# Kernel optimization log

Measured on AMD Instinct MI355X. Metric: run time of the kernel, lower is better.

## Reference

```python
import jax, jax.numpy as jnp
import numpy as np

N_HEAD = 16
D_HEAD = 64


def setup_inputs() -> dict:
    key = jax.random.key(0)
    k1, k2, k3, k4 = jax.random.split(key, 4)
    T, B, D = 1024, 8, 1024
    input = jax.random.normal(k1, (T, B, D), dtype=jnp.float32)
    pos_enc = jax.random.normal(k2, (T, B, D), dtype=jnp.float32) * 0.1
    # causal mask: True = masked (future positions), broadcast over batch
    causal = jnp.triu(jnp.ones((T, T), dtype=bool), k=1)
    attn_mask = jnp.broadcast_to(causal[None, :, :], (B, T, T))
    W_qkv = jax.random.normal(k3, (D, 3 * N_HEAD * D_HEAD), dtype=jnp.float32) * (D ** -0.5)
    W_o = jax.random.normal(k4, (N_HEAD * D_HEAD, N_HEAD * D_HEAD), dtype=jnp.float32) * ((N_HEAD * D_HEAD) ** -0.5)
    return {"input": input, "pos_enc": pos_enc, "attn_mask": attn_mask,
            "W_qkv": W_qkv, "W_o": W_o}


def reference(input, pos_enc, attn_mask, W_qkv, W_o):
    T, B, D = input.shape
    scale = 1.0 / (D_HEAD ** 0.5)
    # attn_type == 2: qkv on (w + r)
    heads = (input + pos_enc) @ W_qkv                      # [T,B,3*n*d]
    q, k, v = jnp.split(heads, 3, axis=-1)
    q = q.reshape(T, B, N_HEAD, D_HEAD)
    k = k.reshape(T, B, N_HEAD, D_HEAD)
    v = v.reshape(T, B, N_HEAD, D_HEAD)
    # scores [B, n, qlen, klen]
    score = jnp.einsum('ibnd,jbnd->bnij', q, k) * scale
    score = jnp.where(attn_mask[:, None, :, :], -jnp.inf, score)
    prob = jax.nn.softmax(score.astype(jnp.float32), axis=-1)  # [B,n,i,j]
    # coverage: mean over heads -> [B,i,j], then transpose -> [B,j,i]
    coverage = jnp.mean(prob, axis=1).transpose(0, 2, 1)
    # dropout is identity at eval (dropatt=0)
    attn_vec = jnp.einsum('bnij,jbnd->ibnd', prob, v)       # [T,B,n,d]
    attn_vec = attn_vec.reshape(T, B, N_HEAD * D_HEAD)
    attn_out = attn_vec @ W_o
    return attn_out, coverage
```

## Files before the change

### kernel.cpp

```cpp
#include <hip/hip_runtime.h>
#include <hip/hip_bf16.h>


typedef __bf16 v8bf __attribute__((ext_vector_type(8)));
typedef float  v4f  __attribute__((ext_vector_type(4)));
typedef unsigned short v8us __attribute__((ext_vector_type(8)));

#define MFMA16x16x32(a, b, c) __builtin_amdgcn_mfma_f32_16x16x32_bf16(a, b, c, 0, 0, 0)

#define GLD_LDS16(g, l) \
    __builtin_amdgcn_global_load_lds((const __attribute__((address_space(1))) void*)(g), \
                                     (__attribute__((address_space(3))) void*)(l), 16, 0, 0)

__device__ __forceinline__ unsigned short f2bf(float f) {
    unsigned int u = __float_as_uint(f);
    u = (u + 0x7FFF + ((u >> 16) & 1)) >> 16;
    return (unsigned short)u;
}

__global__ __launch_bounds__(256) void prep_x(const float* __restrict__ in,
                                              const float* __restrict__ pe,
                                              unsigned short* __restrict__ x) {
    size_t idx = ((size_t)blockIdx.x * 256 + threadIdx.x) * 8;
    v4f a0 = *(const v4f*)(in + idx);
    v4f a1 = *(const v4f*)(in + idx + 4);
    v4f p0 = *(const v4f*)(pe + idx);
    v4f p1 = *(const v4f*)(pe + idx + 4);
    v8us r;
    unsigned short* rp = (unsigned short*)&r;
#pragma unroll
    for (int q = 0; q < 4; q++) {
        rp[q]     = f2bf(a0[q] + p0[q]);
        rp[q + 4] = f2bf(a1[q] + p1[q]);
    }
    *(v8us*)(x + idx) = r;
}

__global__ __launch_bounds__(256) void transpose_f32_bf16(const float* __restrict__ src,
                                                          unsigned short* __restrict__ dst,
                                                          int R, int C) {
    __shared__ alignas(16) unsigned short t[64][72];
    int c0 = blockIdx.x * 64, r0 = blockIdx.y * 64;
    int tid = threadIdx.x;
    int rr = tid >> 2, cg = (tid & 3) * 16;
    const float* s = src + (size_t)(r0 + rr) * C + c0 + cg;
#pragma unroll
    for (int q4 = 0; q4 < 4; q4++) {
        v4f v = *(const v4f*)(s + q4 * 4);
#pragma unroll
        for (int q = 0; q < 4; q++) t[rr][cg + q4 * 4 + q] = f2bf(v[q]);
    }
    __syncthreads();
    v8us o0, o1;
    unsigned short* o0p = (unsigned short*)&o0;
    unsigned short* o1p = (unsigned short*)&o1;
#pragma unroll
    for (int q = 0; q < 8; q++) {
        o0p[q] = t[cg + q][rr];
        o1p[q] = t[cg + 8 + q][rr];
    }
    *(v8us*)(dst + (size_t)(c0 + rr) * R + r0 + cg)     = o0;
    *(v8us*)(dst + (size_t)(c0 + rr) * R + r0 + cg + 8) = o1;
}

__global__ __launch_bounds__(256) void transpose_v(const unsigned short* __restrict__ heads,
                                                   unsigned short* __restrict__ Vt) {
    __shared__ alignas(16) unsigned short t[64][72];
    const int bn = blockIdx.y, b = bn >> 4, n = bn & 15;
    const int j0 = blockIdx.x * 64;
    const int tid = threadIdx.x;
    const int jr = tid >> 2, dg = (tid & 3) * 16;
    const unsigned short* s = heads + ((size_t)(j0 + jr) * 8 + b) * 3072 + 2048 + n * 64 + dg;
    *(v8us*)&t[jr][dg]     = *(const v8us*)(s);
    *(v8us*)&t[jr][dg + 8] = *(const v8us*)(s + 8);
    __syncthreads();
    const int dr = tid >> 2, jg = (tid & 3) * 16;
    v8us o0, o1;
    unsigned short* o0p = (unsigned short*)&o0;
    unsigned short* o1p = (unsigned short*)&o1;
#pragma unroll
    for (int q = 0; q < 8; q++) {
        o0p[q] = t[jg + q][dr];
        o1p[q] = t[jg + 8 + q][dr];
    }
    unsigned short* d = Vt + ((size_t)bn * 64 + dr) * 1024 + j0 + jg;
    *(v8us*)(d)     = o0;
    *(v8us*)(d + 8) = o1;
}

template <bool F32OUT>
__global__ __launch_bounds__(256) void gemm_bf16_v2(const unsigned short* __restrict__ A,
                                                    const unsigned short* __restrict__ Bt,
                                                    void* __restrict__ Cout,
                                                    int M, int N, int K) {
    __shared__ alignas(16) unsigned short As[128 * 64];
    __shared__ alignas(16) unsigned short Bs[128 * 64];

    const int nwgx = gridDim.x;
    const int id   = blockIdx.y * nwgx + blockIdx.x;
    const int cpx  = (nwgx * gridDim.y) >> 3;
    const int id2  = (id & 7) * cpx + (id >> 3);
    const int m0 = (id2 / nwgx) * 128, n0 = (id2 % nwgx) * 128;

    const int tid = threadIdx.x;
    const int lane = tid & 63, wave = tid >> 6;
    const int quad = lane >> 4, lq = lane & 15, lq7 = lq & 7;
    const int mW = (wave & 1) * 64, nW = (wave >> 1) * 64;

    v4f acc[4][4];
#pragma unroll
    for (int mi = 0; mi < 4; mi++)
#pragma unroll
        for (int ni = 0; ni < 4; ni++) acc[mi][ni] = (v4f){0.f, 0.f, 0.f, 0.f};

    const int lr = lane >> 3, lu = lane & 7;
    const int ug = lu ^ lr;
    const unsigned short* agl = A  + (size_t)(m0 + wave * 32 + lr) * K + ug * 8;
    const unsigned short* bgl = Bt + (size_t)(n0 + wave * 32 + lr) * K + ug * 8;
    unsigned short* AsW = (unsigned short*)As + wave * 32 * 64;
    unsigned short* BsW = (unsigned short*)Bs + wave * 32 * 64;

    for (int k0 = 0; k0 < K; k0 += 64) {
        __syncthreads();
#pragma unroll
        for (int t = 0; t < 4; t++) {
            GLD_LDS16(agl + k0 + (size_t)t * 8 * K, AsW + t * 512);
            GLD_LDS16(bgl + k0 + (size_t)t * 8 * K, BsW + t * 512);
        }
        __syncthreads();
#pragma unroll
        for (int h = 0; h < 2; h++) {
            v8bf af[4], bfr[4];
#pragma unroll
            for (int mi = 0; mi < 4; mi++)
                af[mi] = *(const v8bf*)&As[(mW + mi * 16 + lq) * 64 + (((quad + 4 * h) ^ lq7) * 8)];
#pragma unroll
            for (int ni = 0; ni < 4; ni++)
                bfr[ni] = *(const v8bf*)&Bs[(nW + ni * 16 + lq) * 64 + (((quad + 4 * h) ^ lq7) * 8)];
#pragma unroll
            for (int mi = 0; mi < 4; mi++)
#pragma unroll
                for (int ni = 0; ni < 4; ni++)
                    acc[mi][ni] = MFMA16x16x32(af[mi], bfr[ni], acc[mi][ni]);
        }
    }

#pragma unroll
    for (int mi = 0; mi < 4; mi++)
#pragma unroll
        for (int ni = 0; ni < 4; ni++)
#pragma unroll
            for (int r = 0; r < 4; r++) {
                int row = m0 + mW + mi * 16 + quad * 4 + r;
                int col = n0 + nW + ni * 16 + lq;
                if (F32OUT)
                    ((float*)Cout)[(size_t)row * N + col] = acc[mi][ni][r];
                else
                    ((unsigned short*)Cout)[(size_t)row * N + col] = f2bf(acc[mi][ni][r]);
            }
}

#define AT_T  1024
#define AT_B  8
#define AT_NH 16
#define AT_HS 3072
#define AT_ALPHA 0.18033688011112042f

__global__ __launch_bounds__(256) void attn_fused5(const unsigned short* __restrict__ heads,
                                                   const unsigned short* __restrict__ Vt,
                                                   unsigned short* __restrict__ av,
                                                   float* __restrict__ lBuf) {
    __shared__ alignas(16) unsigned short KL[64 * 64];
    __shared__ alignas(16) unsigned short VL[64 * 64];
    __shared__ alignas(16) unsigned short Ps[4 * 16 * 32];
    const int bn = blockIdx.x, b = bn >> 4, n = bn & 15;
    const int y = blockIdx.y;
    const int g = (y < 8) ? (15 - y) : (y - 8);
    const int tid = threadIdx.x;
    const int wv = tid >> 6, lane = tid & 63;
    const int quad = lane >> 4, lq = lane & 15;
    const int i0 = g * 64 + wv * 16;
    const int imax = i0 + 15;

    size_t qbase = ((size_t)(i0 + lq) * 8 + b) * AT_HS + n * 64 + quad * 8;
    v8bf q0 = *(const v8bf*)(heads + qbase);
    v8bf q1 = *(const v8bf*)(heads + qbase + 32);

    const int srow = tid >> 3, sunit = tid & 7;
    const size_t kRowStride = (size_t)8 * AT_HS;
    const unsigned short* kg = heads + ((size_t)srow * 8 + b) * AT_HS + 1024 + n * 64 + sunit * 8;
    const unsigned short* vg = Vt + ((size_t)bn * 64 + srow) * 1024 + sunit * 8;
    const int swz = ((sunit ^ (srow & 7)) * 8);
    unsigned short* kw0 = KL + srow * 64 + swz;
    unsigned short* kw1 = KL + (srow + 32) * 64 + swz;
    unsigned short* vw0 = VL + srow * 64 + swz;
    unsigned short* vw1 = VL + (srow + 32) * 64 + swz;

    v8us kr0 = *(const v8us*)(kg);
    v8us kr1 = *(const v8us*)(kg + 32 * kRowStride);
    v8us vr0 = *(const v8us*)(vg);
    v8us vr1 = *(const v8us*)(vg + 32 * 1024);

    unsigned short* psw = Ps + wv * 512;
    const v8bf* pr = (const v8bf*)(psw + lq * 32 + ((quad ^ (lq & 3)) * 8));
    const int lq7 = lq & 7, lqh = lq >> 3;

    float Sl[4] = {0.f, 0.f, 0.f, 0.f};
    v4f o[4];
#pragma unroll
    for (int dt = 0; dt < 4; dt++) o[dt] = (v4f){0.f, 0.f, 0.f, 0.f};

    for (int c = 0; c <= g; ++c) {
        __syncthreads();
        *(v8us*)kw0 = kr0; *(v8us*)kw1 = kr1;
        *(v8us*)vw0 = vr0; *(v8us*)vw1 = vr1;
        __syncthreads();
        if (c < g) {
            const unsigned short* kgn = kg + (size_t)(c + 1) * 64 * kRowStride;
            kr0 = *(const v8us*)(kgn);
            kr1 = *(const v8us*)(kgn + 32 * kRowStride);
            const unsigned short* vgn = vg + (c + 1) * 64;
            vr0 = *(const v8us*)(vgn);
            vr1 = *(const v8us*)(vgn + 32 * 1024);
        }
        const int jb = c * 64;
#pragma unroll
        for (int jj = 0; jj < 64; jj += 32) {
            const int j0 = jb + jj;
            if (j0 <= imax) {
                const v8bf ka = *(const v8bf*)(KL + (jj + lq) * 64      + ((quad ^ lq7) * 8));
                const v8bf kb = *(const v8bf*)(KL + (jj + lq) * 64      + (((4 + quad) ^ lq7) * 8));
                const v8bf kc = *(const v8bf*)(KL + (jj + 16 + lq) * 64 + ((quad ^ lq7) * 8));
                const v8bf kd = *(const v8bf*)(KL + (jj + 16 + lq) * 64 + (((4 + quad) ^ lq7) * 8));
                v4f s0 = (v4f){0.f, 0.f, 0.f, 0.f}, s1 = s0;
                s0 = MFMA16x16x32(q0, ka, s0);
                s0 = MFMA16x16x32(q1, kb, s0);
                s1 = MFMA16x16x32(q0, kc, s1);
                s1 = MFMA16x16x32(q1, kd, s1);
                const int ja = j0 + lq, jb2 = j0 + 16 + lq;
#pragma unroll
                for (int r = 0; r < 4; ++r) {
                    const int i = i0 + quad * 4 + r;
                    float e0 = exp2f(s0[r] * AT_ALPHA);
                    float e1 = exp2f(s1[r] * AT_ALPHA);
                    float p0 = (ja  <= i) ? e0 : 0.f;
                    float p1 = (jb2 <= i) ? e1 : 0.f;
                    Sl[r] += p0 + p1;
                    psw[(quad * 4 + r) * 32 + ((lqh ^ r) * 8) + lq7]        = f2bf(p0);
                    psw[(quad * 4 + r) * 32 + (((lqh | 2) ^ r) * 8) + lq7]  = f2bf(p1);
                }
                const v8bf pf = *pr;
#pragma unroll
                for (int dt = 0; dt < 4; ++dt) {
                    const v8bf vf = *(const v8bf*)(VL + (dt * 16 + lq) * 64 +
                                                   ((((jj >> 3) + quad) ^ lq7) * 8));
                    o[dt] = MFMA16x16x32(pf, vf, o[dt]);
                }
            }
        }
    }

#pragma unroll
    for (int mask = 1; mask < 16; mask <<= 1)
#pragma unroll
        for (int r = 0; r < 4; r++)
            Sl[r] += __shfl_xor(Sl[r], mask);
    float linv[4];
#pragma unroll
    for (int r = 0; r < 4; r++) linv[r] = __builtin_amdgcn_rcpf(Sl[r]);
    if (lq == 0) {
#pragma unroll
        for (int r = 0; r < 4; r++) {
            int i = i0 + quad * 4 + r;
            lBuf[(size_t)bn * AT_T + i] = Sl[r];
        }
    }
#pragma unroll
    for (int dt = 0; dt < 4; dt++)
#pragma unroll
        for (int r = 0; r < 4; r++) {
            int i = i0 + quad * 4 + r;
            av[((size_t)i * 8 + b) * 1024 + n * 64 + dt * 16 + lq] = f2bf(o[dt][r] * linv[r]);
        }
}

__global__ __launch_bounds__(256) void coverage3(const unsigned short* __restrict__ heads,
                                                 const float* __restrict__ lBuf,
                                                 float* __restrict__ cov) {
    const int jt64 = blockIdx.x, it64 = blockIdx.y, b = blockIdx.z;
    const int i0 = it64 * 64, j0 = jt64 * 64;
    const int tid = threadIdx.x;

    if (jt64 > it64) {
        float* base = cov + (size_t)b * 1048576 + (size_t)(j0 + (tid >> 2)) * 1024
                      + i0 + (tid & 3) * 16;
        v4f z = (v4f){0.f, 0.f, 0.f, 0.f};
#pragma unroll
        for (int q = 0; q < 4; q++) *(v4f*)(base + q * 4) = z;
        return;
    }

    __shared__ alignas(16) char smem[64 * 68 * 4];
    unsigned short* QL = (unsigned short*)smem;
    unsigned short* KL = (unsigned short*)(smem + 8192);
    float* TF = (float*)smem;

    const int wv = tid >> 6, lane = tid & 63;
    const int quad = lane >> 4, lq = lane & 15, lq7 = lq & 7;
    const bool diag = (it64 == jt64);
    const int jtmax = diag ? wv : 3;

    const int srow = tid >> 3, sunit = tid & 7;
    const unsigned short* qgb = heads + ((size_t)(i0 + srow) * 8 + b) * AT_HS + sunit * 8;
    const unsigned short* kgb = heads + ((size_t)(j0 + srow) * 8 + b) * AT_HS + 1024 + sunit * 8;
    const int rowOff32 = 32 * 8 * AT_HS;
    const int swz = (sunit ^ (srow & 7)) * 8;
    unsigned short* qw0 = QL + srow * 64 + swz;
    unsigned short* qw1 = QL + (srow + 32) * 64 + swz;
    unsigned short* kw0 = KL + srow * 64 + swz;
    unsigned short* kw1 = KL + (srow + 32) * 64 + swz;

    v8us qr0 = *(const v8us*)(qgb);
    v8us qr1 = *(const v8us*)(qgb + rowOff32);
    v8us kr0 = *(const v8us*)(kgb);
    v8us kr1 = *(const v8us*)(kgb + rowOff32);

    v4f acc[4];
#pragma unroll
    for (int jt = 0; jt < 4; jt++) acc[jt] = (v4f){0.f, 0.f, 0.f, 0.f};

    const float* lrow = lBuf + (size_t)b * 16 * AT_T + i0 + wv * 16 + quad * 4;

    for (int n = 0; n < 16; ++n) {
        __syncthreads();
        *(v8us*)qw0 = qr0; *(v8us*)qw1 = qr1;
        *(v8us*)kw0 = kr0; *(v8us*)kw1 = kr1;
        __syncthreads();
        if (n < 15) {
            qr0 = *(const v8us*)(qgb + (n + 1) * 64);
            qr1 = *(const v8us*)(qgb + (n + 1) * 64 + rowOff32);
            kr0 = *(const v8us*)(kgb + (n + 1) * 64);
            kr1 = *(const v8us*)(kgb + (n + 1) * 64 + rowOff32);
        }
        v4f lv = *(const v4f*)(lrow + (size_t)n * AT_T);
        float linv[4];
#pragma unroll
        for (int r = 0; r < 4; r++) linv[r] = __builtin_amdgcn_rcpf(lv[r]);

        const v8bf qa = *(const v8bf*)(QL + (wv * 16 + lq) * 64 + ((quad ^ lq7) * 8));
        const v8bf qb = *(const v8bf*)(QL + (wv * 16 + lq) * 64 + (((4 + quad) ^ lq7) * 8));
#pragma unroll
        for (int jt = 0; jt < 4; jt++) {
            if (jt <= jtmax) {
                const v8bf ka = *(const v8bf*)(KL + (jt * 16 + lq) * 64 + ((quad ^ lq7) * 8));
                const v8bf kb = *(const v8bf*)(KL + (jt * 16 + lq) * 64 + (((4 + quad) ^ lq7) * 8));
                v4f s = (v4f){0.f, 0.f, 0.f, 0.f};
                s = MFMA16x16x32(qa, ka, s);
                s = MFMA16x16x32(qb, kb, s);
#pragma unroll
                for (int r = 0; r < 4; r++) {
                    float e = exp2f(s[r] * AT_ALPHA);
                    if (diag && jt == wv && lq > quad * 4 + r) e = 0.f;
                    acc[jt][r] = fmaf(e, linv[r], acc[jt][r]);
                }
            }
        }
    }

    __syncthreads();
#pragma unroll
    for (int jt = 0; jt < 4; jt++) {
        v4f w = acc[jt] * 0.0625f;
        *(v4f*)(TF + (size_t)(jt * 16 + lq) * 68 + wv * 16 + quad * 4) = w;
    }
    __syncthreads();
    {
        const int jl = tid >> 2, cg = (tid & 3) * 16;
        float* dst = cov + (size_t)b * 1048576 + (size_t)(j0 + jl) * 1024 + i0 + cg;
        const float* src = TF + (size_t)jl * 68 + cg;
#pragma unroll
        for (int q = 0; q < 4; q++) *(v4f*)(dst + q * 4) = *(const v4f*)(src + q * 4);
    }
}

extern "C" void kernel_launch(void* const* d_in, const int* in_sizes, int n_in,
                              void* d_out, int out_size, void* d_ws, size_t ws_size,
                              hipStream_t stream) {
    const float* input = (const float*)d_in[0];
    const float* pos   = (const float*)d_in[1];
    const float* Wqkv  = (const float*)d_in[3];
    const float* Wo    = (const float*)d_in[4];
    float* out = (float*)d_out;

    char* ws = (char*)d_ws;
    if (ws_size < 93323264) return;
    unsigned short* x     = (unsigned short*)(ws);
    unsigned short* heads = (unsigned short*)(ws + 16777216);
    unsigned short* av    = (unsigned short*)(ws + 67108864);
    unsigned short* WqkvT = (unsigned short*)(ws + 83886080);
    unsigned short* WoT   = (unsigned short*)(ws + 90177536);
    float* lBuf = (float*)(ws + 92798976);
    unsigned short* Vt = x;

    prep_x<<<4096, 256, 0, stream>>>(input, pos, x);
    transpose_f32_bf16<<<dim3(48, 16), 256, 0, stream>>>(Wqkv, WqkvT, 1024, 3072);
    transpose_f32_bf16<<<dim3(16, 16), 256, 0, stream>>>(Wo, WoT, 1024, 1024);
    gemm_bf16_v2<false><<<dim3(24, 64), 256, 0, stream>>>(x, WqkvT, heads, 8192, 3072, 1024);
    transpose_v<<<dim3(16, 128), 256, 0, stream>>>(heads, Vt);
    attn_fused5<<<dim3(128, 16), 256, 0, stream>>>(heads, Vt, av, lBuf);
    coverage3<<<dim3(16, 16, 8), 256, 0, stream>>>(heads, lBuf, out + 8388608);
    gemm_bf16_v2<true><<<dim3(8, 64), 256, 0, stream>>>(av, WoT, out, 8192, 1024, 1024);
}
```

Measured before the change: 337.8 us.

## Use 256x256 double-buffered GEMM tile for QKV projection

Adds a new GEMM kernel with 256x256 output tiles, 512 threads and double-buffered LDS staging through direct global-to-LDS loads, and uses it for the QKV projection. The larger tile raises arithmetic intensity and cuts redundant global loads, and double-buffering overlaps the next K-tile load with the MFMA work. In exchange it uses 128KB of LDS per block and many accumulator registers, which lowers occupancy. The grid also shrinks to 384 blocks, which may leave CUs unevenly loaded.

Result: slower. 350.9 us (+3.9%).

```diff
diff --git a/kernel.cpp b/kernel.cpp
--- a/kernel.cpp
+++ b/kernel.cpp
@@ -89,6 +89,113 @@
 }
 
 template <bool F32OUT>
+__global__ __launch_bounds__(512, 2) void gemm_bf16_256(const unsigned short* __restrict__ A,
+                                                        const unsigned short* __restrict__ Bt,
+                                                        void* __restrict__ Cout,
+                                                        int M, int N, int K) {
+    __shared__ alignas(16) unsigned short As[2][256 * 64];
+    __shared__ alignas(16) unsigned short Bs[2][256 * 64];
+
+    const int nwgx = gridDim.x;
+    const int id   = blockIdx.y * nwgx + blockIdx.x;
+    const int cpx  = (nwgx * gridDim.y) >> 3;
+    const int id2  = (id & 7) * cpx + (id >> 3);
+    const int m0 = (id2 / nwgx) * 256, n0 = (id2 % nwgx) * 256;
+
+    const int tid = threadIdx.x;
+    const int wv = tid >> 6, lane = tid & 63;
+    const int wm = wv >> 2, wn = wv & 3;
+    const int quad = lane >> 4, lq = lane & 15, lq7 = lq & 7;
+
+    v4f acc[8][4];
+#pragma unroll
+    for (int mf = 0; mf < 8; mf++)
+#pragma unroll
+        for (int nf = 0; nf < 4; nf++) acc[mf][nf] = (v4f){0.f, 0.f, 0.f, 0.f};
+
+    const int lr = lane >> 3, lu = lane & 7;
+    const int ug = lu ^ lr;
+    const unsigned short* agl = A  + (size_t)(m0 + wv * 32 + lr) * K + ug * 8;
+    const unsigned short* bgl = Bt + (size_t)(n0 + wv * 32 + lr) * K + ug * 8;
+
+#define STAGE256(buf, kk)                                                          \
+    do {                                                                           \
+        _Pragma("unroll")                                                          \
+        for (int t = 0; t < 4; t++) {                                              \
+            GLD_LDS16(agl + (size_t)(kk) * 64 + (size_t)t * 8 * K,                 \
+                      &As[buf][(wv * 32 + t * 8) * 64]);                           \
+            GLD_LDS16(bgl + (size_t)(kk) * 64 + (size_t)t * 8 * K,                 \
+                      &Bs[buf][(wv * 32 + t * 8) * 64]);                           \
+        }                                                                          \
+    } while (0)
+
+    const int NT = K >> 6;
+    STAGE256(0, 0);
+    STAGE256(1, 1);
+
+    for (int t2 = 0; t2 < NT; ++t2) {
+        const int c = t2 & 1;
+        if (t2 + 1 < NT) asm volatile("s_waitcnt vmcnt(8)" ::: "memory");
+        else             asm volatile("s_waitcnt vmcnt(0)" ::: "memory");
+        __builtin_amdgcn_sched_barrier(0);
+        __builtin_amdgcn_s_barrier();
+        __builtin_amdgcn_sched_barrier(0);
+
+#pragma unroll
+        for (int qm = 0; qm < 2; qm++) {
+            v8bf af[4][2];
+#pragma unroll
+            for (int mf = 0; mf < 4; mf++)
+#pragma unroll
+                for (int kh = 0; kh < 2; kh++)
+                    af[mf][kh] = *(const v8bf*)&As[c][(wm * 128 + (qm * 4 + mf) * 16 + lq) * 64 +
+                                                      (((kh * 4 + quad) ^ lq7) * 8)];
+#pragma unroll
+            for (int qn = 0; qn < 2; qn++) {
+                v8bf bfr[2][2];
+#pragma unroll
+                for (int nf = 0; nf < 2; nf++)
+#pragma unroll
+                    for (int kh = 0; kh < 2; kh++)
+                        bfr[nf][kh] = *(const v8bf*)&Bs[c][(wn * 64 + (qn * 2 + nf) * 16 + lq) * 64 +
+                                                           (((kh * 4 + quad) ^ lq7) * 8)];
+                __builtin_amdgcn_s_setprio(1);
+#pragma unroll
+                for (int mf = 0; mf < 4; mf++)
+#pragma unroll
+                    for (int nf = 0; nf < 2; nf++)
+#pragma unroll
+                        for (int kh = 0; kh < 2; kh++)
+                            acc[qm * 4 + mf][qn * 2 + nf] =
+                                MFMA16x16x32(af[mf][kh], bfr[nf][kh], acc[qm * 4 + mf][qn * 2 + nf]);
+                __builtin_amdgcn_s_setprio(0);
+            }
+        }
+
+        asm volatile("" ::: "memory");
+        __builtin_amdgcn_sched_barrier(0);
+        __builtin_amdgcn_s_barrier();
+        __builtin_amdgcn_sched_barrier(0);
+        if (t2 + 2 < NT) STAGE256(c, t2 + 2);
+    }
+
+#pragma unroll
+    for (int mf = 0; mf < 8; mf++)
+#pragma unroll
+        for (int nf = 0; nf < 4; nf++)
+#pragma unroll
+            for (int r = 0; r < 4; r++) {
+                int row = m0 + wm * 128 + mf * 16 + quad * 4 + r;
+                int col = n0 + wn * 64 + nf * 16 + lq;
+                if (F32OUT)
+                    ((float*)Cout)[(size_t)row * N + col] = acc[mf][nf][r];
+                else
+                    ((unsigned short*)Cout)[(size_t)row * N + col] = f2bf(acc[mf][nf][r]);
+            }
+#undef STAGE256
+}
+
+template <bool F32OUT>
 __global__ __launch_bounds__(256) void gemm_bf16_v2(const unsigned short* __restrict__ A,
                                                     const unsigned short* __restrict__ Bt,
                                                     void* __restrict__ Cout,
@@ -405,7 +512,7 @@
     prep_x<<<4096, 256, 0, stream>>>(input, pos, x);
     transpose_f32_bf16<<<dim3(48, 16), 256, 0, stream>>>(Wqkv, WqkvT, 1024, 3072);
     transpose_f32_bf16<<<dim3(16, 16), 256, 0, stream>>>(Wo, WoT, 1024, 1024);
-    gemm_bf16_v2<false><<<dim3(24, 64), 256, 0, stream>>>(x, WqkvT, heads, 8192, 3072, 1024);
+    gemm_bf16_256<false><<<dim3(12, 32), 512, 0, stream>>>(x, WqkvT, heads, 8192, 3072, 1024);
     transpose_v<<<dim3(16, 128), 256, 0, stream>>>(heads, Vt);
     attn_fused5<<<dim3(128, 16), 256, 0, stream>>>(heads, Vt, av, lBuf);
     coverage3<<<dim3(16, 16, 8), 256, 0, stream>>>(heads, lBuf, out + 8388608);
```

## Merge prep kernels into one launch and co-schedule coverage with output GEMM

Applied to the files above, without the earlier changes.

Three preprocessing kernels (input+pos cast, two weight transposes) are merged into one launch that dispatches on block index. The coverage kernel and the final W_o GEMM become a single launch, with blocks partitioned by flat index. The goal is to cut launch overhead and fill idle CUs during the lightly loaded coverage tail by running the independent GEMM work at the same time. In exchange, the combined kernel carries the larger of the two register and LDS footprints, which may lower occupancy for the coverage blocks.

Result: slower. 353.5 us (+4.6%).

```diff
diff --git a/kernel.cpp b/kernel.cpp
--- a/kernel.cpp
+++ b/kernel.cpp
@@ -18,30 +18,11 @@
     return (unsigned short)u;
 }
 
-__global__ __launch_bounds__(256) void prep_x(const float* __restrict__ in,
-                                              const float* __restrict__ pe,
-                                              unsigned short* __restrict__ x) {
-    size_t idx = ((size_t)blockIdx.x * 256 + threadIdx.x) * 8;
-    v4f a0 = *(const v4f*)(in + idx);
-    v4f a1 = *(const v4f*)(in + idx + 4);
-    v4f p0 = *(const v4f*)(pe + idx);
-    v4f p1 = *(const v4f*)(pe + idx + 4);
-    v8us r;
-    unsigned short* rp = (unsigned short*)&r;
-#pragma unroll
-    for (int q = 0; q < 4; q++) {
-        rp[q]     = f2bf(a0[q] + p0[q]);
-        rp[q + 4] = f2bf(a1[q] + p1[q]);
-    }
-    *(v8us*)(x + idx) = r;
-}
-
-__global__ __launch_bounds__(256) void transpose_f32_bf16(const float* __restrict__ src,
-                                                          unsigned short* __restrict__ dst,
-                                                          int R, int C) {
-    __shared__ alignas(16) unsigned short t[64][72];
-    int c0 = blockIdx.x * 64, r0 = blockIdx.y * 64;
-    int tid = threadIdx.x;
+__device__ __forceinline__ void transpose_tile_f32_bf16(const float* __restrict__ src,
+                                                        unsigned short* __restrict__ dst,
+                                                        int R, int C, int bx, int by,
+                                                        int tid, unsigned short (*t)[72]) {
+    int c0 = bx * 64, r0 = by * 64;
     int rr = tid >> 2, cg = (tid & 3) * 16;
     const float* s = src + (size_t)(r0 + rr) * C + c0 + cg;
 #pragma unroll
@@ -61,6 +42,38 @@
     }
     *(v8us*)(dst + (size_t)(c0 + rr) * R + r0 + cg)     = o0;
     *(v8us*)(dst + (size_t)(c0 + rr) * R + r0 + cg + 8) = o1;
+}
+
+__global__ __launch_bounds__(256) void prep_all(const float* __restrict__ in,
+                                                const float* __restrict__ pe,
+                                                unsigned short* __restrict__ x,
+                                                const float* __restrict__ Wqkv,
+                                                unsigned short* __restrict__ WqkvT,
+                                                const float* __restrict__ Wo,
+                                                unsigned short* __restrict__ WoT) {
+    __shared__ alignas(16) unsigned short t[64][72];
+    const int id = blockIdx.x, tid = threadIdx.x;
+    if (id < 4096) {
+        size_t idx = ((size_t)id * 256 + tid) * 8;
+        v4f a0 = *(const v4f*)(in + idx);
+        v4f a1 = *(const v4f*)(in + idx + 4);
+        v4f p0 = *(const v4f*)(pe + idx);
+        v4f p1 = *(const v4f*)(pe + idx + 4);
+        v8us r;
+        unsigned short* rp = (unsigned short*)&r;
+#pragma unroll
+        for (int q = 0; q < 4; q++) {
+            rp[q]     = f2bf(a0[q] + p0[q]);
+            rp[q + 4] = f2bf(a1[q] + p1[q]);
+        }
+        *(v8us*)(x + idx) = r;
+    } else if (id < 4864) {
+        int r = id - 4096;
+        transpose_tile_f32_bf16(Wqkv, WqkvT, 1024, 3072, r % 48, r / 48, tid, t);
+    } else {
+        int r = id - 4864;
+        transpose_tile_f32_bf16(Wo, WoT, 1024, 1024, r % 16, r / 16, tid, t);
+    }
 }
 
 __global__ __launch_bounds__(256) void transpose_v(const unsigned short* __restrict__ heads,
@@ -284,102 +297,171 @@
         }
 }
 
-__global__ __launch_bounds__(256) void coverage3(const unsigned short* __restrict__ heads,
-                                                 const float* __restrict__ lBuf,
-                                                 float* __restrict__ cov) {
-    const int jt64 = blockIdx.x, it64 = blockIdx.y, b = blockIdx.z;
-    const int i0 = it64 * 64, j0 = jt64 * 64;
-    const int tid = threadIdx.x;
-
-    if (jt64 > it64) {
-        float* base = cov + (size_t)b * 1048576 + (size_t)(j0 + (tid >> 2)) * 1024
-                      + i0 + (tid & 3) * 16;
-        v4f z = (v4f){0.f, 0.f, 0.f, 0.f};
-#pragma unroll
-        for (int q = 0; q < 4; q++) *(v4f*)(base + q * 4) = z;
-        return;
-    }
-
-    __shared__ alignas(16) char smem[64 * 68 * 4];
-    unsigned short* QL = (unsigned short*)smem;
-    unsigned short* KL = (unsigned short*)(smem + 8192);
-    float* TF = (float*)smem;
-
-    const int wv = tid >> 6, lane = tid & 63;
-    const int quad = lane >> 4, lq = lane & 15, lq7 = lq & 7;
-    const bool diag = (it64 == jt64);
-    const int jtmax = diag ? wv : 3;
-
-    const int srow = tid >> 3, sunit = tid & 7;
-    const unsigned short* qgb = heads + ((size_t)(i0 + srow) * 8 + b) * AT_HS + sunit * 8;
-    const unsigned short* kgb = heads + ((size_t)(j0 + srow) * 8 + b) * AT_HS + 1024 + sunit * 8;
-    const int rowOff32 = 32 * 8 * AT_HS;
-    const int swz = (sunit ^ (srow & 7)) * 8;
-    unsigned short* qw0 = QL + srow * 64 + swz;
-    unsigned short* qw1 = QL + (srow + 32) * 64 + swz;
-    unsigned short* kw0 = KL + srow * 64 + swz;
-    unsigned short* kw1 = KL + (srow + 32) * 64 + swz;
-
-    v8us qr0 = *(const v8us*)(qgb);
-    v8us qr1 = *(const v8us*)(qgb + rowOff32);
-    v8us kr0 = *(const v8us*)(kgb);
-    v8us kr1 = *(const v8us*)(kgb + rowOff32);
-
-    v4f acc[4];
-#pragma unroll
-    for (int jt = 0; jt < 4; jt++) acc[jt] = (v4f){0.f, 0.f, 0.f, 0.f};
-
-    const float* lrow = lBuf + (size_t)b * 16 * AT_T + i0 + wv * 16 + quad * 4;
-
-    for (int n = 0; n < 16; ++n) {
-        __syncthreads();
-        *(v8us*)qw0 = qr0; *(v8us*)qw1 = qr1;
-        *(v8us*)kw0 = kr0; *(v8us*)kw1 = kr1;
-        __syncthreads();
-        if (n < 15) {
-            qr0 = *(const v8us*)(qgb + (n + 1) * 64);
-            qr1 = *(const v8us*)(qgb + (n + 1) * 64 + rowOff32);
-            kr0 = *(const v8us*)(kgb + (n + 1) * 64);
-            kr1 = *(const v8us*)(kgb + (n + 1) * 64 + rowOff32);
-        }
-        v4f lv = *(const v4f*)(lrow + (size_t)n * AT_T);
-        float linv[4];
-#pragma unroll
-        for (int r = 0; r < 4; r++) linv[r] = __builtin_amdgcn_rcpf(lv[r]);
-
-        const v8bf qa = *(const v8bf*)(QL + (wv * 16 + lq) * 64 + ((quad ^ lq7) * 8));
-        const v8bf qb = *(const v8bf*)(QL + (wv * 16 + lq) * 64 + (((4 + quad) ^ lq7) * 8));
+__global__ __launch_bounds__(256) void cov_wo(const unsigned short* __restrict__ heads,
+                                              const float* __restrict__ lBuf,
+                                              float* __restrict__ cov,
+                                              const unsigned short* __restrict__ av,
+                                              const unsigned short* __restrict__ WoT,
+                                              float* __restrict__ outO) {
+    __shared__ alignas(16) char smem[32768];
+    const int flat = blockIdx.x, tid = threadIdx.x;
+
+    if (flat < 2048) {
+        const int jt64 = flat & 15, it64 = (flat >> 4) & 15, b = flat >> 8;
+        const int i0 = it64 * 64, j0 = jt64 * 64;
+
+        if (jt64 > it64) {
+            float* base = cov + (size_t)b * 1048576 + (size_t)(j0 + (tid >> 2)) * 1024
+                          + i0 + (tid & 3) * 16;
+            v4f z = (v4f){0.f, 0.f, 0.f, 0.f};
+#pragma unroll
+            for (int q = 0; q < 4; q++) *(v4f*)(base + q * 4) = z;
+            return;
+        }
+
+        unsigned short* QL = (unsigned short*)smem;
+        unsigned short* KL = (unsigned short*)(smem + 8192);
+        float* TF = (float*)smem;
+
+        const int wv = tid >> 6, lane = tid & 63;
+        const int quad = lane >> 4, lq = lane & 15, lq7 = lq & 7;
+        const bool diag = (it64 == jt64);
+        const int jtmax = diag ? wv : 3;
+
+        const int srow = tid >> 3, sunit = tid & 7;
+        const unsigned short* qgb = heads + ((size_t)(i0 + srow) * 8 + b) * AT_HS + sunit * 8;
+        const unsigned short* kgb = heads + ((size_t)(j0 + srow) * 8 + b) * AT_HS + 1024 + sunit * 8;
+        const int rowOff32 = 32 * 8 * AT_HS;
+        const int swz = (sunit ^ (srow & 7)) * 8;
+        unsigned short* qw0 = QL + srow * 64 + swz;
+        unsigned short* qw1 = QL + (srow + 32) * 64 + swz;
+        unsigned short* kw0 = KL + srow * 64 + swz;
+        unsigned short* kw1 = KL + (srow + 32) * 64 + swz;
+
+        v8us qr0 = *(const v8us*)(qgb);
+        v8us qr1 = *(const v8us*)(qgb + rowOff32);
+        v8us kr0 = *(const v8us*)(kgb);
+        v8us kr1 = *(const v8us*)(kgb + rowOff32);
+
+        v4f acc[4];
+#pragma unroll
+        for (int jt = 0; jt < 4; jt++) acc[jt] = (v4f){0.f, 0.f, 0.f, 0.f};
+
+        const float* lrow = lBuf + (size_t)b * 16 * AT_T + i0 + wv * 16 + quad * 4;
+
+        for (int n = 0; n < 16; ++n) {
+            __syncthreads();
+            *(v8us*)qw0 = qr0; *(v8us*)qw1 = qr1;
+            *(v8us*)kw0 = kr0; *(v8us*)kw1 = kr1;
+            __syncthreads();
+            if (n < 15) {
+                qr0 = *(const v8us*)(qgb + (n + 1) * 64);
+                qr1 = *(const v8us*)(qgb + (n + 1) * 64 + rowOff32);
+                kr0 = *(const v8us*)(kgb + (n + 1) * 64);
+                kr1 = *(const v8us*)(kgb + (n + 1) * 64 + rowOff32);
+            }
+            v4f lv = *(const v4f*)(lrow + (size_t)n * AT_T);
+            float linv[4];
+#pragma unroll
+            for (int r = 0; r < 4; r++) linv[r] = __builtin_amdgcn_rcpf(lv[r]);
+
+            const v8bf qa = *(const v8bf*)(QL + (wv * 16 + lq) * 64 + ((quad ^ lq7) * 8));
+            const v8bf qb = *(const v8bf*)(QL + (wv * 16 + lq) * 64 + (((4 + quad) ^ lq7) * 8));
+#pragma unroll
+            for (int jt = 0; jt < 4; jt++) {
+                if (jt <= jtmax) {
+                    const v8bf ka = *(const v8bf*)(KL + (jt * 16 + lq) * 64 + ((quad ^ lq7) * 8));
+                    const v8bf kb = *(const v8bf*)(KL + (jt * 16 + lq) * 64 + (((4 + quad) ^ lq7) * 8));
+                    v4f s = (v4f){0.f, 0.f, 0.f, 0.f};
+                    s = MFMA16x16x32(qa, ka, s);
+                    s = MFMA16x16x32(qb, kb, s);
+#pragma unroll
+                    for (int r = 0; r < 4; r++) {
+                        float e = exp2f(s[r] * AT_ALPHA);
+                        if (diag && jt == wv && lq > quad * 4 + r) e = 0.f;
+                        acc[jt][r] = fmaf(e, linv[r], acc[jt][r]);
+                    }
+                }
+            }
+        }
+
+        __syncthreads();
 #pragma unroll
         for (int jt = 0; jt < 4; jt++) {
-            if (jt <= jtmax) {
-                const v8bf ka = *(const v8bf*)(KL + (jt * 16 + lq) * 64 + ((quad ^ lq7) * 8));
-                const v8bf kb = *(const v8bf*)(KL + (jt * 16 + lq) * 64 + (((4 + quad) ^ lq7) * 8));
-                v4f s = (v4f){0.f, 0.f, 0.f, 0.f};
-                s = MFMA16x16x32(qa, ka, s);
-                s = MFMA16x16x32(qb, kb, s);
+            v4f w = acc[jt] * 0.0625f;
+            *(v4f*)(TF + (size_t)(jt * 16 + lq) * 68 + wv * 16 + quad * 4) = w;
+        }
+        __syncthreads();
+        {
+            const int jl = tid >> 2, cg = (tid & 3) * 16;
+            float* dst = cov + (size_t)b * 1048576 + (size_t)(j0 + jl) * 1024 + i0 + cg;
+            const float* src = TF + (size_t)jl * 68 + cg;
+#pragma unroll
+            for (int q = 0; q < 4; q++) *(v4f*)(dst + q * 4) = *(const v4f*)(src + q * 4);
+        }
+    } else {
+        const int M = 8192, N = 1024, K = 1024;
+        unsigned short* As = (unsigned short*)smem;
+        unsigned short* Bs = (unsigned short*)(smem + 16384);
+
+        const int nwgx = 8;
+        const int id   = flat - 2048;
+        const int cpx  = 512 >> 3;
+        const int id2  = (id & 7) * cpx + (id >> 3);
+        const int m0 = (id2 / nwgx) * 128, n0 = (id2 % nwgx) * 128;
+
+        const int lane = tid & 63, wave = tid >> 6;
+        const int quad = lane >> 4, lq = lane & 15, lq7 = lq & 7;
+        const int mW = (wave & 1) * 64, nW = (wave >> 1) * 64;
+
+        v4f acc[4][4];
+#pragma unroll
+        for (int mi = 0; mi < 4; mi++)
+#pragma unroll
+            for (int ni = 0; ni < 4; ni++) acc[mi][ni] = (v4f){0.f, 0.f, 0.f, 0.f};
+
+        const int lr = lane >> 3, lu = lane & 7;
+        const int ug = lu ^ lr;
+        const unsigned short* agl = av  + (size_t)(m0 + wave * 32 + lr) * K + ug * 8;
+        const unsigned short* bgl = WoT + (size_t)(n0 + wave * 32 + lr) * K + ug * 8;
+        unsigned short* AsW = As + wave * 32 * 64;
+        unsigned short* BsW = Bs + wave * 32 * 64;
+
+        for (int k0 = 0; k0 < K; k0 += 64) {
+            __syncthreads();
+#pragma unroll
+            for (int t = 0; t < 4; t++) {
+                GLD_LDS16(agl + k0 + (size_t)t * 8 * K, AsW + t * 512);
+                GLD_LDS16(bgl + k0 + (size_t)t * 8 * K, BsW + t * 512);
+            }
+            __syncthreads();
+#pragma unroll
+            for (int h = 0; h < 2; h++) {
+                v8bf af[4], bfr[4];
+#pragma unroll
+                for (int mi = 0; mi < 4; mi++)
+                    af[mi] = *(const v8bf*)&As[(mW + mi * 16 + lq) * 64 + (((quad + 4 * h) ^ lq7) * 8)];
+#pragma unroll
+                for (int ni = 0; ni < 4; ni++)
+                    bfr[ni] = *(const v8bf*)&Bs[(nW + ni * 16 + lq) * 64 + (((quad + 4 * h) ^ lq7) * 8)];
+#pragma unroll
+                for (int mi = 0; mi < 4; mi++)
+#pragma unroll
+                    for (int ni = 0; ni < 4; ni++)
+                        acc[mi][ni] = MFMA16x16x32(af[mi], bfr[ni], acc[mi][ni]);
+            }
+        }
+
+#pragma unroll
+        for (int mi = 0; mi < 4; mi++)
+#pragma unroll
+            for (int ni = 0; ni < 4; ni++)
 #pragma unroll
                 for (int r = 0; r < 4; r++) {
-                    float e = exp2f(s[r] * AT_ALPHA);
-                    if (diag && jt == wv && lq > quad * 4 + r) e = 0.f;
-                    acc[jt][r] = fmaf(e, linv[r], acc[jt][r]);
+                    int row = m0 + mW + mi * 16 + quad * 4 + r;
+                    int col = n0 + nW + ni * 16 + lq;
+                    outO[(size_t)row * N + col] = acc[mi][ni][r];
                 }
-            }
-        }
-    }
-
-    __syncthreads();
-#pragma unroll
-    for (int jt = 0; jt < 4; jt++) {
-        v4f w = acc[jt] * 0.0625f;
-        *(v4f*)(TF + (size_t)(jt * 16 + lq) * 68 + wv * 16 + quad * 4) = w;
-    }
-    __syncthreads();
-    {
-        const int jl = tid >> 2, cg = (tid & 3) * 16;
-        float* dst = cov + (size_t)b * 1048576 + (size_t)(j0 + jl) * 1024 + i0 + cg;
-        const float* src = TF + (size_t)jl * 68 + cg;
-#pragma unroll
-        for (int q = 0; q < 4; q++) *(v4f*)(dst + q * 4) = *(const v4f*)(src + q * 4);
     }
 }
 
@@ -402,12 +484,9 @@
     float* lBuf = (float*)(ws + 92798976);
     unsigned short* Vt = x;
 
-    prep_x<<<4096, 256, 0, stream>>>(input, pos, x);
-    transpose_f32_bf16<<<dim3(48, 16), 256, 0, stream>>>(Wqkv, WqkvT, 1024, 3072);
-    transpose_f32_bf16<<<dim3(16, 16), 256, 0, stream>>>(Wo, WoT, 1024, 1024);
+    prep_all<<<5120, 256, 0, stream>>>(input, pos, x, Wqkv, WqkvT, Wo, WoT);
     gemm_bf16_v2<false><<<dim3(24, 64), 256, 0, stream>>>(x, WqkvT, heads, 8192, 3072, 1024);
     transpose_v<<<dim3(16, 128), 256, 0, stream>>>(heads, Vt);
     attn_fused5<<<dim3(128, 16), 256, 0, stream>>>(heads, Vt, av, lBuf);
-    coverage3<<<dim3(16, 16, 8), 256, 0, stream>>>(heads, lBuf, out + 8388608);
-    gemm_bf16_v2<true><<<dim3(8, 64), 256, 0, stream>>>(av, WoT, out, 8192, 1024, 1024);
-}
+    cov_wo<<<2560, 256, 0, stream>>>(heads, lBuf, out + 8388608, av, WoT, out);
+}
```

## Split coverage kernel over head quarters with atomic accumulation, zero output in prep

Applied to the files above, without the earlier changes.

The coverage kernel is split along heads into four groups, each block handling four heads, so the grid grows fourfold and more work runs in parallel. Partial sums are combined into the coverage output with per-element atomicAdd. This needs the output zeroed first, so extra blocks appended to prep_x clear the whole coverage buffer. The costs are the Q/K tile reloads and per-head setup repeated per split, plus scalar atomic traffic in place of vectorized stores.

Result: slower. 1.162 ms (+243.8%).

```diff
diff --git a/kernel.cpp b/kernel.cpp
--- a/kernel.cpp
+++ b/kernel.cpp
@@ -20,8 +20,17 @@
 
 __global__ __launch_bounds__(256) void prep_x(const float* __restrict__ in,
                                               const float* __restrict__ pe,
-                                              unsigned short* __restrict__ x) {
-    size_t idx = ((size_t)blockIdx.x * 256 + threadIdx.x) * 8;
+                                              unsigned short* __restrict__ x,
+                                              float* __restrict__ cz) {
+    const int id = blockIdx.x, tid = threadIdx.x;
+    if (id >= 4096) {
+        float* base = cz + (size_t)(id - 4096) * 16384 + (tid << 2);
+        v4f z = (v4f){0.f, 0.f, 0.f, 0.f};
+#pragma unroll
+        for (int k = 0; k < 16; k++) *(v4f*)(base + k * 1024) = z;
+        return;
+    }
+    size_t idx = ((size_t)id * 256 + tid) * 8;
     v4f a0 = *(const v4f*)(in + idx);
     v4f a1 = *(const v4f*)(in + idx + 4);
     v4f p0 = *(const v4f*)(pe + idx);
@@ -284,21 +293,14 @@
         }
 }
 
-__global__ __launch_bounds__(256) void coverage3(const unsigned short* __restrict__ heads,
+__global__ __launch_bounds__(256) void coverage6(const unsigned short* __restrict__ heads,
                                                  const float* __restrict__ lBuf,
                                                  float* __restrict__ cov) {
-    const int jt64 = blockIdx.x, it64 = blockIdx.y, b = blockIdx.z;
+    const int jt64 = blockIdx.x, it64 = blockIdx.y;
+    const int b = blockIdx.z >> 2, nq = blockIdx.z & 3;
+    if (jt64 > it64) return;
     const int i0 = it64 * 64, j0 = jt64 * 64;
     const int tid = threadIdx.x;
-
-    if (jt64 > it64) {
-        float* base = cov + (size_t)b * 1048576 + (size_t)(j0 + (tid >> 2)) * 1024
-                      + i0 + (tid & 3) * 16;
-        v4f z = (v4f){0.f, 0.f, 0.f, 0.f};
-#pragma unroll
-        for (int q = 0; q < 4; q++) *(v4f*)(base + q * 4) = z;
-        return;
-    }
 
     __shared__ alignas(16) char smem[64 * 68 * 4];
     unsigned short* QL = (unsigned short*)smem;
@@ -320,10 +322,12 @@
     unsigned short* kw0 = KL + srow * 64 + swz;
     unsigned short* kw1 = KL + (srow + 32) * 64 + swz;
 
-    v8us qr0 = *(const v8us*)(qgb);
-    v8us qr1 = *(const v8us*)(qgb + rowOff32);
-    v8us kr0 = *(const v8us*)(kgb);
-    v8us kr1 = *(const v8us*)(kgb + rowOff32);
+    const int nbase = nq * 4;
+
+    v8us qr0 = *(const v8us*)(qgb + nbase * 64);
+    v8us qr1 = *(const v8us*)(qgb + nbase * 64 + rowOff32);
+    v8us kr0 = *(const v8us*)(kgb + nbase * 64);
+    v8us kr1 = *(const v8us*)(kgb + nbase * 64 + rowOff32);
 
     v4f acc[4];
 #pragma unroll
@@ -331,12 +335,14 @@
 
     const float* lrow = lBuf + (size_t)b * 16 * AT_T + i0 + wv * 16 + quad * 4;
 
-    for (int n = 0; n < 16; ++n) {
+#pragma unroll
+    for (int h = 0; h < 4; ++h) {
+        const int n = nbase + h;
         __syncthreads();
         *(v8us*)qw0 = qr0; *(v8us*)qw1 = qr1;
         *(v8us*)kw0 = kr0; *(v8us*)kw1 = kr1;
         __syncthreads();
-        if (n < 15) {
+        if (h < 3) {
             qr0 = *(const v8us*)(qgb + (n + 1) * 64);
             qr1 = *(const v8us*)(qgb + (n + 1) * 64 + rowOff32);
             kr0 = *(const v8us*)(kgb + (n + 1) * 64);
@@ -379,7 +385,7 @@
         float* dst = cov + (size_t)b * 1048576 + (size_t)(j0 + jl) * 1024 + i0 + cg;
         const float* src = TF + (size_t)jl * 68 + cg;
 #pragma unroll
-        for (int q = 0; q < 4; q++) *(v4f*)(dst + q * 4) = *(const v4f*)(src + q * 4);
+        for (int q = 0; q < 16; q++) atomicAdd(dst + q, src[q]);
     }
 }
 
@@ -402,12 +408,14 @@
     float* lBuf = (float*)(ws + 92798976);
     unsigned short* Vt = x;
 
-    prep_x<<<4096, 256, 0, stream>>>(input, pos, x);
+    float* cov = out + 8388608;
+
+    prep_x<<<4608, 256, 0, stream>>>(input, pos, x, cov);
     transpose_f32_bf16<<<dim3(48, 16), 256, 0, stream>>>(Wqkv, WqkvT, 1024, 3072);
     transpose_f32_bf16<<<dim3(16, 16), 256, 0, stream>>>(Wo, WoT, 1024, 1024);
     gemm_bf16_v2<false><<<dim3(24, 64), 256, 0, stream>>>(x, WqkvT, heads, 8192, 3072, 1024);
     transpose_v<<<dim3(16, 128), 256, 0, stream>>>(heads, Vt);
     attn_fused5<<<dim3(128, 16), 256, 0, stream>>>(heads, Vt, av, lBuf);
-    coverage3<<<dim3(16, 16, 8), 256, 0, stream>>>(heads, lBuf, out + 8388608);
+    coverage6<<<dim3(16, 16, 32), 256, 0, stream>>>(heads, lBuf, cov);
     gemm_bf16_v2<true><<<dim3(8, 64), 256, 0, stream>>>(av, WoT, out, 8192, 1024, 1024);
 }
```
